# Kernel tuning notes

Measured on AMD Instinct MI355X. Metric: run time of the kernel, lower is better.

## Reference

```python
import jax, jax.numpy as jnp
import numpy as np

EPS = 1e-5  # BatchNorm eps (torch default)

def _bn(x, gamma, beta):
    # training-mode BatchNorm over the edge/node (leading) axis, biased var
    mean = x.mean(axis=0, keepdims=True)
    var = x.var(axis=0, keepdims=True)
    return (x - mean) * jax.lax.rsqrt(var + EPS) * gamma + beta

def _silu(x):
    return x * jax.nn.sigmoid(x)

def setup_inputs() -> dict:
    N, E, H, NH = 50000, 800000, 128, 4
    HD = H // NH
    key = jax.random.key(0)
    ks = jax.random.split(key, 8)
    x = jax.random.normal(ks[0], (N, H), dtype=jnp.float32)
    weight = jax.random.uniform(ks[1], (N, 1), dtype=jnp.float32)  # positive fraction weights
    src = jax.random.randint(ks[2], (E,), 0, N)
    dst = jax.random.randint(ks[3], (E,), 0, N)
    # f: Linear(2H, 1) + BN(1)
    Wf = jax.random.normal(ks[4], (2 * H, 1), dtype=jnp.float32) * 0.05
    bf = jnp.zeros((1,), jnp.float32)
    f_gamma = jnp.ones((1,), jnp.float32)
    f_beta = jnp.zeros((1,), jnp.float32)
    # g: NH heads of Linear(2H, HD) + BN(HD), stacked on leading head axis
    Wg = jax.random.normal(ks[5], (NH, 2 * H, HD), dtype=jnp.float32) * 0.05
    bg = jnp.zeros((NH, HD), jnp.float32)
    g_gamma = jnp.ones((NH, HD), jnp.float32)
    g_beta = jnp.zeros((NH, HD), jnp.float32)
    # bn_nodes: BN(H)
    n_gamma = jnp.ones((H,), jnp.float32)
    n_beta = jnp.zeros((H,), jnp.float32)
    return dict(x=x, weight=weight, src=src, dst=dst, Wf=Wf, bf=bf,
                f_gamma=f_gamma, f_beta=f_beta, Wg=Wg, bg=bg,
                g_gamma=g_gamma, g_beta=g_beta, n_gamma=n_gamma, n_beta=n_beta)

def reference(x, weight, src, dst, Wf, bf, f_gamma, f_beta, Wg, bg, g_gamma, g_beta, n_gamma, n_beta):
    N = x.shape[0]
    E = src.shape[0]
    # per-edge concat of src/dst node features: [E, 2H]
    hihj = jnp.concatenate([x[src], x[dst]], axis=-1)
    # attention logit f(hihj) = SiLU(BN(Linear)) then exp: [E, 1]
    exp_e = jnp.exp(_silu(_bn(hihj @ Wf + bf, f_gamma, f_beta)))
    # weighted softmax-like normalization over incoming edges of each dst node
    we = weight[src] * exp_e                                   # [E, 1]
    sum_w_exp = jax.ops.segment_sum(we, dst, num_segments=N)   # [N, 1]
    a = we / sum_w_exp[dst]                                    # [E, 1]
    # multi-head message: a_ij * SiLU(BN(Linear_h(hihj))) per head, concat
    z = jnp.einsum('ed,hdk->ehk', hihj, Wg) + bg               # [E, NH, HD]
    z = _silu(_bn(z, g_gamma, g_beta))
    msg = (a[:, :, None] * z).reshape(E, -1)                   # [E, H]
    h = jax.ops.segment_sum(msg, dst, num_segments=N)          # [N, H]
    out = _bn(h, n_gamma, n_beta) + x                          # residual
    return out
```

## Files before the change

### kernel.cpp

```cpp
#include <hip/hip_runtime.h>
#include <hip/hip_bf16.h>
#include <math.h>

#define HDIM 128
#define PAD 64
typedef unsigned short ushort_t;
typedef unsigned int uint_t;
typedef __attribute__((ext_vector_type(8))) short bf16x8;
typedef __attribute__((ext_vector_type(4))) float f32x4;
typedef __attribute__((ext_vector_type(2))) float v2f;

__device__ __forceinline__ float wave_allreduce(float v){
  #pragma unroll
  for (int o = 1; o < 64; o <<= 1) v += __shfl_xor(v, o);
  return v;
}

__device__ __forceinline__ ushort_t f2bf(float f){
  uint_t u = __float_as_uint(f);
  uint_t r = (u + 0x7fffu + ((u >> 16) & 1u)) >> 16;
  return (ushort_t)r;
}

__device__ __forceinline__ v2f bf2(uint_t u){
  v2f r;
  r.x = __uint_as_float(u << 16);
  r.y = __uint_as_float(u & 0xffff0000u);
  return r;
}

__global__ __launch_bounds__(128) void k_wpack(const float* __restrict__ Wg,
    const float* __restrict__ Wf, ushort_t* __restrict__ W3,
    int* __restrict__ cnt, int C){
  int b = blockIdx.x;
  int k = threadIdx.x;
  if (b < 272){
    float val;
    if (b < 128)       val = Wg[(size_t)(b >> 5) * 8192 + k * 32 + (b & 31)];
    else if (b < 256){ int c2 = b - 128;
                       val = Wg[(size_t)(c2 >> 5) * 8192 + (k + 128) * 32 + (c2 & 31)]; }
    else if (b == 256) val = Wf[k];
    else if (b == 257) val = Wf[128 + k];
    else               val = 0.f;
    int idx = (((b >> 4) * 4 + (k >> 5)) * 16 + (b & 15)) * 32 + (k & 31);
    W3[idx] = f2bf(val);
  } else {
    int i = (b - 272) * 128 + k;
    if (i < C) cnt[i] = 0;
  }
}

__global__ __launch_bounds__(256) void k_gemmfill(const float* __restrict__ x,
    const ushort_t* __restrict__ W3, const float* __restrict__ weight,
    ushort_t* __restrict__ Pb, ushort_t* __restrict__ Qb,
    float* __restrict__ v, float2* __restrict__ uw2,
    const int* __restrict__ src, const int* __restrict__ dst,
    int* __restrict__ cnt, int* __restrict__ es,
    int N, int E, int FB){
  __shared__ ushort_t xl[32 * 128];
  __shared__ ushort_t cl[32 * 264];
  if ((int)blockIdx.x < FB){
    int t = blockIdx.x * 256 + threadIdx.x;
    int e0 = t * 8;
#define FILL1(d, s) { \
    int c = atomicAdd(&cnt[d], 1); \
    if (c < PAD) es[(size_t)(d) * PAD + c] = (s); }
    if (e0 + 8 <= E){
      int4 da = *(const int4*)(dst + e0);
      int4 db = *(const int4*)(dst + e0 + 4);
      int4 sa = *(const int4*)(src + e0);
      int4 sb = *(const int4*)(src + e0 + 4);
      FILL1(da.x, sa.x) FILL1(da.y, sa.y) FILL1(da.z, sa.z) FILL1(da.w, sa.w)
      FILL1(db.x, sb.x) FILL1(db.y, sb.y) FILL1(db.z, sb.z) FILL1(db.w, sb.w)
    } else {
      for (int e = e0; e < E; ++e){
        int d = dst[e];
        FILL1(d, src[e])
      }
    }
#undef FILL1
  } else {
    int tid = threadIdx.x;
    int n_base = ((int)blockIdx.x - FB) * 32;
    #pragma unroll
    for (int i = 0; i < 4; ++i){
      int cidx = i * 256 + tid;
      int row = cidx >> 5, ch = cidx & 31;
      int rowc = n_base + row; rowc = rowc < N ? rowc : N - 1;
      float4 a = *(const float4*)(x + (size_t)rowc * HDIM + ch * 4);
      uint_t lo = (uint_t)f2bf(a.x) | ((uint_t)f2bf(a.y) << 16);
      uint_t hi = (uint_t)f2bf(a.z) | ((uint_t)f2bf(a.w) << 16);
      int bo = (row * 256 + ch * 8) ^ ((row & 7) << 4);
      *(uint2*)((char*)xl + bo) = make_uint2(lo, hi);
    }
    __syncthreads();
    int wid = __builtin_amdgcn_readfirstlane(tid >> 6);
    int lane = tid & 63;
    int quad = lane >> 4, col = lane & 15;
    int strip = wid >> 1;
    int half = wid & 1;
    int tbeg = half * 8;
    int ntile = half ? 9 : 8;
    f32x4 acc[9];
    #pragma unroll
    for (int t = 0; t < 9; ++t) acc[t] = (f32x4){0.f, 0.f, 0.f, 0.f};
    int arow = strip * 16 + col;
    #pragma unroll
    for (int kk = 0; kk < 4; ++kk){
      int abyte = (arow * 256 + kk * 64 + quad * 16) ^ ((col & 7) << 4);
      bf16x8 af = *(const bf16x8*)((char*)xl + abyte);
      const ushort_t* wb = W3 + (size_t)(tbeg * 4 + kk) * 512 + col * 32 + quad * 8;
      #pragma unroll
      for (int t = 0; t < 9; ++t){
        if (t < ntile){
          bf16x8 bfr = *(const bf16x8*)(wb + (size_t)t * 2048);
          acc[t] = __builtin_amdgcn_mfma_f32_16x16x32_bf16(af, bfr, acc[t], 0, 0, 0);
        }
      }
    }
    #pragma unroll
    for (int t = 0; t < 8; ++t){
      int ct = tbeg + t;
      #pragma unroll
      for (int r = 0; r < 4; ++r){
        int lr = strip * 16 + quad * 4 + r;
        cl[lr * 264 + ct * 16 + col] = f2bf(acc[t][r]);
      }
    }
    if (half){
      #pragma unroll
      for (int r = 0; r < 4; ++r){
        int n = n_base + strip * 16 + quad * 4 + r;
        if (n < N){
          float val = acc[8][r];
          if (col == 0)      uw2[n] = make_float2(val, weight[n]);
          else if (col == 1) v[n] = val;
        }
      }
    }
    __syncthreads();
    int row = tid >> 3, seg = tid & 7;
    int n = n_base + row;
    if (n < N){
      const ushort_t* s = cl + row * 264 + seg * 32;
      uint4 w0 = *(const uint4*)(s);
      uint4 w1 = *(const uint4*)(s + 8);
      uint4 w2 = *(const uint4*)(s + 16);
      uint4 w3v = *(const uint4*)(s + 24);
      if (seg < 4){
        ushort_t* dp = Pb + (size_t)n * HDIM + seg * 32;
        *(uint4*)(dp) = w0; *(uint4*)(dp + 8) = w1;
        *(uint4*)(dp + 16) = w2; *(uint4*)(dp + 24) = w3v;
      } else {
        ushort_t* dp = Qb + (size_t)n * HDIM + (seg - 4) * 32;
        *(uint4*)(dp) = w0; *(uint4*)(dp + 8) = w1;
        *(uint4*)(dp + 16) = w2; *(uint4*)(dp + 24) = w3v;
      }
    }
  }
}

#define SH8(sjv,jj,S) \
  int S##0=__shfl(sjv,(jj)),   S##1=__shfl(sjv,(jj)+1), S##2=__shfl(sjv,(jj)+2), S##3=__shfl(sjv,(jj)+3), \
      S##4=__shfl(sjv,(jj)+4), S##5=__shfl(sjv,(jj)+5), S##6=__shfl(sjv,(jj)+6), S##7=__shfl(sjv,(jj)+7);
#define LD8(S,P) \
  uint_t P##0=Pu[(size_t)S##0*64+lane], P##1=Pu[(size_t)S##1*64+lane], \
         P##2=Pu[(size_t)S##2*64+lane], P##3=Pu[(size_t)S##3*64+lane], \
         P##4=Pu[(size_t)S##4*64+lane], P##5=Pu[(size_t)S##5*64+lane], \
         P##6=Pu[(size_t)S##6*64+lane], P##7=Pu[(size_t)S##7*64+lane];
#define SH4(sjv,jj,S) \
  int S##0=__shfl(sjv,(jj)),   S##1=__shfl(sjv,(jj)+1), S##2=__shfl(sjv,(jj)+2), S##3=__shfl(sjv,(jj)+3);
#define LD4(S,P) \
  uint_t P##0=Pu[(size_t)S##0*64+lane], P##1=Pu[(size_t)S##1*64+lane], \
         P##2=Pu[(size_t)S##2*64+lane], P##3=Pu[(size_t)S##3*64+lane];

__global__ __launch_bounds__(256) void k_gstats(const ushort_t* __restrict__ Pb,
    const ushort_t* __restrict__ Qb, const float* __restrict__ v,
    const float2* __restrict__ uw2, const int* __restrict__ es,
    const int* __restrict__ cnt, float* __restrict__ pstatG, int N){
  int lane = threadIdx.x & 63;
  int wid = __builtin_amdgcn_readfirstlane(threadIdx.x >> 6);
  int part = (int)blockIdx.x & 7;
  int Npp = (N + 7) >> 3;
  int lo = part * Npp;
  int hi = lo + Npp; if (hi > N) hi = N;
  int stp = (gridDim.x >> 3) << 2;
  const uint_t* Pu = (const uint_t*)Pb;
  const uint_t* Qu = (const uint_t*)Qb;
  v2f gs = {0.f,0.f}, gq = {0.f,0.f};
  float fs = 0.f, fq = 0.f;
  int n0 = lo + ((blockIdx.x >> 3) << 2) + wid;
  int n1 = n0 + stp;
  int dnA=0,sjA=0; uint_t qAu=0; float vA=0.f;
  int dnB=0,sjB=0; uint_t qBu=0; float vB=0.f;
  if (n0 < hi){ dnA=cnt[n0]; sjA=es[(size_t)n0*PAD+lane];
                qAu=Qu[(size_t)n0*64+lane]; vA=v[n0]; }
  if (n1 < hi){ dnB=cnt[n1]; sjB=es[(size_t)n1*PAD+lane];
                qBu=Qu[(size_t)n1*64+lane]; vB=v[n1]; }
#define GST(p,Sv,Qv) { v2f y=bf2(p); Sv+=y; Qv.x=fmaf(y.x,y.x,Qv.x); Qv.y=fmaf(y.y,y.y,Qv.y); }
#define GED8(P,Sv,Qv) GST(P##0,Sv,Qv) GST(P##1,Sv,Qv) GST(P##2,Sv,Qv) GST(P##3,Sv,Qv) \
                      GST(P##4,Sv,Qv) GST(P##5,Sv,Qv) GST(P##6,Sv,Qv) GST(P##7,Sv,Qv)
#define GED4(P,Sv,Qv) GST(P##0,Sv,Qv) GST(P##1,Sv,Qv) GST(P##2,Sv,Qv) GST(P##3,Sv,Qv)
  while (n0 < hi){
    int m0 = n0 + 2*stp, m1 = n1 + 2*stp;
    int dnC=0,sjC=0; uint_t qCu=0; float vC=0.f;
    int dnD=0,sjD=0; uint_t qDu=0; float vD=0.f;
    if (m0 < hi){ dnC=cnt[m0]; sjC=es[(size_t)m0*PAD+lane];
                  qCu=Qu[(size_t)m0*64+lane]; vC=v[m0]; }
    if (m1 < hi){ dnD=cnt[m1]; sjD=es[(size_t)m1*PAD+lane];
                  qDu=Qu[(size_t)m1*64+lane]; vD=v[m1]; }
    int dA = dnA < PAD ? dnA : PAD;
    int dB = (n1 < hi) ? (dnB < PAD ? dnB : PAD) : 0;
    if (lane < dA){ float2 uw = uw2[sjA]; float t = uw.x + vA; fs += t; fq = fmaf(t,t,fq); }
    if (lane < dB){ float2 uw = uw2[sjB]; float t = uw.x + vB; fs += t; fq = fmaf(t,t,fq); }
    v2f qa = bf2(qAu), qb = bf2(qBu);
    v2f SnA={0.f,0.f}, SSA={0.f,0.f}, SnB={0.f,0.f}, SSB={0.f,0.f};
    int j0 = 0, j1 = 0;
    for (; j0 + 7 < dA && j1 + 7 < dB; j0 += 8, j1 += 8){
      SH8(sjA,j0,xa) SH8(sjB,j1,xb)
      LD8(xa,pa) LD8(xb,pb)
      GED8(pa,SnA,SSA) GED8(pb,SnB,SSB)
    }
    for (; j0 + 7 < dA; j0 += 8){ SH8(sjA,j0,xa) LD8(xa,pa) GED8(pa,SnA,SSA) }
    for (; j0 + 3 < dA; j0 += 4){ SH4(sjA,j0,xa) LD4(xa,pa) GED4(pa,SnA,SSA) }
    for (; j0 < dA; ++j0){ int s0=__shfl(sjA,j0); uint_t p0=Pu[(size_t)s0*64+lane]; GST(p0,SnA,SSA) }
    for (; j1 + 7 < dB; j1 += 8){ SH8(sjB,j1,xb) LD8(xb,pb) GED8(pb,SnB,SSB) }
    for (; j1 + 3 < dB; j1 += 4){ SH4(sjB,j1,xb) LD4(xb,pb) GED4(pb,SnB,SSB) }
    for (; j1 < dB; ++j1){ int s0=__shfl(sjB,j1); uint_t p0=Pu[(size_t)s0*64+lane]; GST(p0,SnB,SSB) }
    float dAf = (float)dA, dBf = (float)dB;
    gs.x += SnA.x + SnB.x + dAf*qa.x + dBf*qb.x;
    gs.y += SnA.y + SnB.y + dAf*qa.y + dBf*qb.y;
    gq.x += SSA.x + SSB.x + qa.x*fmaf(dAf,qa.x,2.f*SnA.x) + qb.x*fmaf(dBf,qb.x,2.f*SnB.x);
    gq.y += SSA.y + SSB.y + qa.y*fmaf(dAf,qa.y,2.f*SnA.y) + qb.y*fmaf(dBf,qb.y,2.f*SnB.y);
    n0 = m0; n1 = m1;
    dnA=dnC; sjA=sjC; qAu=qCu; vA=vC;
    dnB=dnD; sjB=sjD; qBu=qDu; vB=vD;
  }
#undef GST
#undef GED8
#undef GED4
  fs = wave_allreduce(fs); fq = wave_allreduce(fq);
  __shared__ float red[4][258];
  red[wid][2*lane]       = gs.x; red[wid][2*lane+1]   = gs.y;
  red[wid][128+2*lane]   = gq.x; red[wid][129+2*lane] = gq.y;
  if (lane == 0){ red[wid][256] = fs; red[wid][257] = fq; }
  __syncthreads();
  for (int c = threadIdx.x; c < 258; c += 256)
    pstatG[(size_t)blockIdx.x * 258 + c] = red[0][c] + red[1][c] + red[2][c] + red[3][c];
}

__global__ __launch_bounds__(256) void k_redfin1(const float* __restrict__ pstatG,
    int NB, const float* __restrict__ g_gamma, const float* __restrict__ g_beta,
    const float* __restrict__ f_gamma, const float* __restrict__ f_beta,
    float* __restrict__ fin, long long E){
  int j = blockIdx.x;
  int c1 = (j < 128) ? j : 256;
  int c2 = (j < 128) ? 128 + j : 257;
  double s1 = 0, s2 = 0;
  for (int b = threadIdx.x; b < NB; b += 256){
    const float* pb = pstatG + (size_t)b * 258;
    s1 += (double)pb[c1]; s2 += (double)pb[c2];
  }
  __shared__ double m1[256], m2[256];
  m1[threadIdx.x] = s1; m2[threadIdx.x] = s2;
  __syncthreads();
  for (int o = 128; o; o >>= 1){
    if (threadIdx.x < o){ m1[threadIdx.x] += m1[threadIdx.x + o];
                          m2[threadIdx.x] += m2[threadIdx.x + o]; }
    __syncthreads();
  }
  if (threadIdx.x == 0){
    double m = m1[0] / (double)E;
    double var = m2[0] / (double)E - m * m;
    if (j < 128){
      float sc = (float)((double)g_gamma[j] / sqrt(var + 1e-5));
      fin[2 + j] = sc; fin[130 + j] = g_beta[j] - (float)m * sc;
    } else {
      float sc = (float)((double)f_gamma[0] / sqrt(var + 1e-5));
      fin[0] = sc; fin[1] = f_beta[0] - (float)m * sc;
    }
  }
}

__global__ __launch_bounds__(256) void k_msg(const ushort_t* __restrict__ Pb,
    const ushort_t* __restrict__ Qb, const float* __restrict__ v,
    const float2* __restrict__ uw2, const int* __restrict__ es,
    const int* __restrict__ cnt, const float* __restrict__ fin,
    float* __restrict__ h, float* __restrict__ pstatH, int N){
  int lane = threadIdx.x & 63;
  int wid = __builtin_amdgcn_readfirstlane(threadIdx.x >> 6);
  int part = (int)blockIdx.x & 7;
  int Npp = (N + 7) >> 3;
  int lo = part * Npp;
  int hi = lo + Npp; if (hi > N) hi = N;
  int stp = (gridDim.x >> 3) << 2;
  const uint_t* Pu = (const uint_t*)Pb;
  const uint_t* Qu = (const uint_t*)Qb;
  float fsc = fin[0], fsh = fin[1];
  v2f gsc = {fin[2 + 2*lane], fin[3 + 2*lane]};
  v2f gsh = {fin[130 + 2*lane], fin[131 + 2*lane]};
  v2f hs = {0.f,0.f}, hq = {0.f,0.f};
  int n0 = lo + ((blockIdx.x >> 3) << 2) + wid;
  int n1 = n0 + stp;
  int dnA=0,sjA=0; uint_t qAu=0; float vA=0.f;
  int dnB=0,sjB=0; uint_t qBu=0; float vB=0.f;
  if (n0 < hi){ dnA=cnt[n0]; sjA=es[(size_t)n0*PAD+lane];
                qAu=Qu[(size_t)n0*64+lane]; vA=v[n0]; }
  if (n1 < hi){ dnB=cnt[n1]; sjB=es[(size_t)n1*PAD+lane];
                qBu=Qu[(size_t)n1*64+lane]; vB=v[n1]; }
#define EDGE(p,a,qv,av) { v2f y = (bf2(p) + qv) * gsc + gsh; \
      float e0 = __expf(-y.x), e1 = __expf(-y.y); \
      float d0 = 1.f + e0, d1 = 1.f + e1; \
      float r = __builtin_amdgcn_rcpf(d0 * d1) * (a); \
      av.x = fmaf(y.x * d1, r, av.x); av.y = fmaf(y.y * d0, r, av.y); }
#define ASH8(wjv,jj,A) \
  float A##0=__shfl(wjv,(jj)),   A##1=__shfl(wjv,(jj)+1), A##2=__shfl(wjv,(jj)+2), A##3=__shfl(wjv,(jj)+3), \
        A##4=__shfl(wjv,(jj)+4), A##5=__shfl(wjv,(jj)+5), A##6=__shfl(wjv,(jj)+6), A##7=__shfl(wjv,(jj)+7);
#define ASH4(wjv,jj,A) \
  float A##0=__shfl(wjv,(jj)),   A##1=__shfl(wjv,(jj)+1), A##2=__shfl(wjv,(jj)+2), A##3=__shfl(wjv,(jj)+3);
#define MED8(P,A,qv,av) EDGE(P##0,A##0,qv,av) EDGE(P##1,A##1,qv,av) EDGE(P##2,A##2,qv,av) EDGE(P##3,A##3,qv,av) \
                        EDGE(P##4,A##4,qv,av) EDGE(P##5,A##5,qv,av) EDGE(P##6,A##6,qv,av) EDGE(P##7,A##7,qv,av)
#define MED4(P,A,qv,av) EDGE(P##0,A##0,qv,av) EDGE(P##1,A##1,qv,av) EDGE(P##2,A##2,qv,av) EDGE(P##3,A##3,qv,av)
  while (n0 < hi){
    int m0 = n0 + 2*stp, m1 = n1 + 2*stp;
    int dnC=0,sjC=0; uint_t qCu=0; float vC=0.f;
    int dnD=0,sjD=0; uint_t qDu=0; float vD=0.f;
    if (m0 < hi){ dnC=cnt[m0]; sjC=es[(size_t)m0*PAD+lane];
                  qCu=Qu[(size_t)m0*64+lane]; vC=v[m0]; }
    if (m1 < hi){ dnD=cnt[m1]; sjD=es[(size_t)m1*PAD+lane];
                  qDu=Qu[(size_t)m1*64+lane]; vD=v[m1]; }
    int dA = dnA < PAD ? dnA : PAD;
    int dB = (n1 < hi) ? (dnB < PAD ? dnB : PAD) : 0;
    float wjA = 0.f, wjB = 0.f;
    if (lane < dA){ float2 uw = uw2[sjA];
      float tt = fmaf(uw.x + vA, fsc, fsh);
      float sl = tt * __builtin_amdgcn_rcpf(1.f + __expf(-tt));
      wjA = uw.y * __expf(sl); }
    if (lane < dB){ float2 uw = uw2[sjB];
      float tt = fmaf(uw.x + vB, fsc, fsh);
      float sl = tt * __builtin_amdgcn_rcpf(1.f + __expf(-tt));
      wjB = uw.y * __expf(sl); }
    v2f qa = bf2(qAu), qb = bf2(qBu);
    v2f accA = {0.f,0.f}, accB = {0.f,0.f};
    int j0 = 0, j1 = 0;
    for (; j0 + 7 < dA && j1 + 7 < dB; j0 += 8, j1 += 8){
      SH8(sjA,j0,xa) SH8(sjB,j1,xb)
      ASH8(wjA,j0,aa) ASH8(wjB,j1,ab)
      LD8(xa,pa) LD8(xb,pb)
      MED8(pa,aa,qa,accA) MED8(pb,ab,qb,accB)
    }
    for (; j0 + 7 < dA; j0 += 8){ SH8(sjA,j0,xa) ASH8(wjA,j0,aa) LD8(xa,pa) MED8(pa,aa,qa,accA) }
    for (; j0 + 3 < dA; j0 += 4){ SH4(sjA,j0,xa) ASH4(wjA,j0,aa) LD4(xa,pa) MED4(pa,aa,qa,accA) }
    for (; j0 < dA; ++j0){ int s0=__shfl(sjA,j0); float a0=__shfl(wjA,j0);
                           uint_t p0=Pu[(size_t)s0*64+lane]; EDGE(p0,a0,qa,accA) }
    for (; j1 + 7 < dB; j1 += 8){ SH8(sjB,j1,xb) ASH8(wjB,j1,ab) LD8(xb,pb) MED8(pb,ab,qb,accB) }
    for (; j1 + 3 < dB; j1 += 4){ SH4(sjB,j1,xb) ASH4(wjB,j1,ab) LD4(xb,pb) MED4(pb,ab,qb,accB) }
    for (; j1 < dB; ++j1){ int s0=__shfl(sjB,j1); float a0=__shfl(wjB,j1);
                           uint_t p0=Pu[(size_t)s0*64+lane]; EDGE(p0,a0,qb,accB) }
    float swA = wjA, swB = wjB;
    #pragma unroll
    for (int o = 1; o < 64; o <<= 1){ swA += __shfl_xor(swA, o); swB += __shfl_xor(swB, o); }
    float rsA = (dA > 0) ? (1.f / swA) : 0.f;
    float rsB = (dB > 0) ? (1.f / swB) : 0.f;
    accA.x *= rsA; accA.y *= rsA;
    accB.x *= rsB; accB.y *= rsB;
    *(float2*)&h[(size_t)n0 * 128 + 2*lane] = make_float2(accA.x, accA.y);
    hs += accA; hq += accA * accA;
    if (n1 < hi){
      *(float2*)&h[(size_t)n1 * 128 + 2*lane] = make_float2(accB.x, accB.y);
      hs += accB; hq += accB * accB;
    }
    n0 = m0; n1 = m1;
    dnA=dnC; sjA=sjC; qAu=qCu; vA=vC;
    dnB=dnD; sjB=sjD; qBu=qDu; vB=vD;
  }
#undef EDGE
#undef ASH8
#undef ASH4
#undef MED8
#undef MED4
  __shared__ float red[4][256];
  red[wid][2*lane]       = hs.x; red[wid][2*lane+1]   = hs.y;
  red[wid][128+2*lane]   = hq.x; red[wid][129+2*lane] = hq.y;
  __syncthreads();
  int c = threadIdx.x;
  pstatH[(size_t)blockIdx.x * 256 + c] = red[0][c] + red[1][c] + red[2][c] + red[3][c];
}

__global__ __launch_bounds__(256) void k_redfin2(const float* __restrict__ pstatH,
    int NB, const float* __restrict__ n_gamma, const float* __restrict__ n_beta,
    float* __restrict__ fin, int N){
  int j = blockIdx.x;
  double s1 = 0, s2 = 0;
  for (int b = threadIdx.x; b < NB; b += 256){
    const float* pb = pstatH + (size_t)b * 256;
    s1 += (double)pb[j]; s2 += (double)pb[128 + j];
  }
  __shared__ double m1[256], m2[256];
  m1[threadIdx.x] = s1; m2[threadIdx.x] = s2;
  __syncthreads();
  for (int o = 128; o; o >>= 1){
    if (threadIdx.x < o){ m1[threadIdx.x] += m1[threadIdx.x + o];
                          m2[threadIdx.x] += m2[threadIdx.x + o]; }
    __syncthreads();
  }
  if (threadIdx.x == 0){
    double m = m1[0] / (double)N;
    double var = m2[0] / (double)N - m * m;
    float sc = (float)((double)n_gamma[j] / sqrt(var + 1e-5));
    fin[258 + j] = sc; fin[386 + j] = n_beta[j] - (float)m * sc;
  }
}

__global__ __launch_bounds__(256) void k_out(const float* __restrict__ h,
    const float* __restrict__ x, const float* __restrict__ fin,
    float* __restrict__ out, int total4){
  int i = blockIdx.x * 256 + threadIdx.x;
  if (i >= total4) return;
  const float4* h4 = (const float4*)h; const float4* x4 = (const float4*)x;
  float4 hv = h4[i], xv = x4[i];
  int c = (i * 4) & 127;
  float4 o;
  o.x = fmaf(hv.x, fin[258 + c],     fin[386 + c])     + xv.x;
  o.y = fmaf(hv.y, fin[258 + c + 1], fin[386 + c + 1]) + xv.y;
  o.z = fmaf(hv.z, fin[258 + c + 2], fin[386 + c + 2]) + xv.z;
  o.w = fmaf(hv.w, fin[258 + c + 3], fin[386 + c + 3]) + xv.w;
  ((float4*)out)[i] = o;
}

extern "C" void kernel_launch(void* const* d_in, const int* in_sizes, int n_in,
                              void* d_out, int out_size, void* d_ws, size_t ws_size,
                              hipStream_t stream){
  const float* x       = (const float*)d_in[0];
  const float* weight  = (const float*)d_in[1];
  const int*   src     = (const int*)d_in[2];
  const int*   dst     = (const int*)d_in[3];
  const float* Wf      = (const float*)d_in[4];
  const float* f_gamma = (const float*)d_in[6];
  const float* f_beta  = (const float*)d_in[7];
  const float* Wg      = (const float*)d_in[8];
  const float* g_gamma = (const float*)d_in[10];
  const float* g_beta  = (const float*)d_in[11];
  const float* n_gamma = (const float*)d_in[12];
  const float* n_beta  = (const float*)d_in[13];
  float* out = (float*)d_out;

  int N = in_sizes[0] / HDIM;
  int E = in_sizes[2];

  char* ws = (char*)d_ws;
  size_t off = 0;
  auto alloc = [&](size_t bytes)->char*{
    char* p = ws + off; off = (off + bytes + 255) & ~(size_t)255; return p;
  };
  ushort_t* Pb    = (ushort_t*)alloc((size_t)N * HDIM * 2);
  ushort_t* Qb    = (ushort_t*)alloc((size_t)N * HDIM * 2);
  float* h        = (float*)alloc((size_t)N * HDIM * 4);
  float* v        = (float*)alloc((size_t)N * 4);
  float2* uw2     = (float2*)alloc((size_t)N * 8);
  int* es         = (int*)alloc((size_t)N * PAD * 4);
  ushort_t* W3    = (ushort_t*)alloc((size_t)272 * 128 * 2);
  int* cnt        = (int*)alloc((size_t)N * 4);
  const int NWB = 512;
  const int NB  = NWB;
  float*  pstatG = (float*)alloc((size_t)NB * 258 * 4);
  float*  pstatH = (float*)alloc((size_t)NB * 256 * 4);
  float*  fin    = (float*)alloc(514 * 4);

  int GB = (N + 31) / 32;
  int FB = (E + 2047) / 2048;

  k_wpack   <<<272 + (N + 127) / 128, 128, 0, stream>>>(Wg, Wf, W3, cnt, N);
  k_gemmfill<<<FB + GB, 256, 0, stream>>>(x, W3, weight, Pb, Qb, v, uw2,
                                          src, dst, cnt, es, N, E, FB);
  k_gstats  <<<NWB, 256, 0, stream>>>(Pb, Qb, v, uw2, es, cnt, pstatG, N);
  k_redfin1 <<<129, 256, 0, stream>>>(pstatG, NB, g_gamma, g_beta, f_gamma, f_beta, fin, (long long)E);
  k_msg     <<<NWB, 256, 0, stream>>>(Pb, Qb, v, uw2, es, cnt, fin, h, pstatH, N);
  k_redfin2 <<<128, 256, 0, stream>>>(pstatH, NB, n_gamma, n_beta, fin, N);
  k_out     <<<(N * HDIM / 4 + 255) / 256, 256, 0, stream>>>(h, x, fin, out, N * HDIM / 4);
}
```

Measured before the change: 303.1 us.

## Bucket edges by destination block before building per-node adjacency lists

Replaces the per-edge global atomic fill of the padded per-node edge lists with a two-pass bucketing scheme. Edges are first scattered into 256-node buckets using shared-memory histograms and one global atomic per bucket per block. Each bucket is then turned into padded adjacency lists in shared memory and written out densely, which also removes the separate count-zeroing. The goal is to cut global atomic contention and random scattered writes, at the cost of an extra queue buffer, a fixed per-bucket capacity and silent truncation if a bucket overflows. The stats and message kernels also launch with 2048 blocks instead of 512.

```diff
diff --git a/kernel.cpp b/kernel.cpp
--- a/kernel.cpp
+++ b/kernel.cpp
@@ -4,6 +4,7 @@
 
 #define HDIM 128
 #define PAD 64
+#define QCAP 8192
 typedef unsigned short ushort_t;
 typedef unsigned int uint_t;
 typedef __attribute__((ext_vector_type(8))) short bf16x8;
@@ -29,12 +30,14 @@
   return r;
 }
 
-__global__ __launch_bounds__(128) void k_wpack(const float* __restrict__ Wg,
+__global__ __launch_bounds__(256) void k_wpack(const float* __restrict__ Wg,
     const float* __restrict__ Wf, ushort_t* __restrict__ W3,
-    int* __restrict__ cnt, int C){
+    const int* __restrict__ src, const int* __restrict__ dst,
+    uint_t* __restrict__ queue, int* __restrict__ tails, int E){
   int b = blockIdx.x;
-  int k = threadIdx.x;
   if (b < 272){
+    int k = threadIdx.x;
+    if (k >= 128) return;
     float val;
     if (b < 128)       val = Wg[(size_t)(b >> 5) * 8192 + k * 32 + (b & 31)];
     else if (b < 256){ int c2 = b - 128;
@@ -44,44 +47,78 @@
     else               val = 0.f;
     int idx = (((b >> 4) * 4 + (k >> 5)) * 16 + (b & 15)) * 32 + (k & 31);
     W3[idx] = f2bf(val);
+    return;
+  }
+  __shared__ int hist[256], gbase[256];
+  int t = threadIdx.x;
+  hist[t] = 0;
+  __syncthreads();
+  int e0 = ((b - 272) * 256 + t) * 8;
+  int d0=0,d1=0,d2=0,d3=0,d4=0,d5=0,d6=0,d7=0;
+  int s0=0,s1=0,s2=0,s3=0,s4=0,s5=0,s6=0,s7=0;
+  bool v0=e0<E, v1=e0+1<E, v2=e0+2<E, v3=e0+3<E,
+       v4=e0+4<E, v5=e0+5<E, v6=e0+6<E, v7=e0+7<E;
+  if (v7 && (e0 + 8 <= E)){
+    int4 da = *(const int4*)(dst + e0); int4 db_ = *(const int4*)(dst + e0 + 4);
+    int4 sa = *(const int4*)(src + e0); int4 sb_ = *(const int4*)(src + e0 + 4);
+    d0=da.x; d1=da.y; d2=da.z; d3=da.w; d4=db_.x; d5=db_.y; d6=db_.z; d7=db_.w;
+    s0=sa.x; s1=sa.y; s2=sa.z; s3=sa.w; s4=sb_.x; s5=sb_.y; s6=sb_.z; s7=sb_.w;
   } else {
-    int i = (b - 272) * 128 + k;
-    if (i < C) cnt[i] = 0;
-  }
+    if (v0){ d0=dst[e0];   s0=src[e0];   }
+    if (v1){ d1=dst[e0+1]; s1=src[e0+1]; }
+    if (v2){ d2=dst[e0+2]; s2=src[e0+2]; }
+    if (v3){ d3=dst[e0+3]; s3=src[e0+3]; }
+    if (v4){ d4=dst[e0+4]; s4=src[e0+4]; }
+    if (v5){ d5=dst[e0+5]; s5=src[e0+5]; }
+    if (v6){ d6=dst[e0+6]; s6=src[e0+6]; }
+    if (v7){ d7=dst[e0+7]; s7=src[e0+7]; }
+  }
+#define DIST1(i) int b##i = d##i >> 8, r##i = 0; \
+    if (v##i) r##i = atomicAdd(&hist[b##i], 1);
+  DIST1(0) DIST1(1) DIST1(2) DIST1(3) DIST1(4) DIST1(5) DIST1(6) DIST1(7)
+#undef DIST1
+  __syncthreads();
+  if (hist[t]) gbase[t] = atomicAdd(&tails[t], hist[t]);
+  __syncthreads();
+#define DISTW(i) if (v##i){ int q = gbase[b##i] + r##i; if (q < QCAP) \
+    queue[(size_t)b##i * QCAP + q] = ((uint_t)(d##i & 255) << 16) | (uint_t)s##i; }
+  DISTW(0) DISTW(1) DISTW(2) DISTW(3) DISTW(4) DISTW(5) DISTW(6) DISTW(7)
+#undef DISTW
 }
 
 __global__ __launch_bounds__(256) void k_gemmfill(const float* __restrict__ x,
     const ushort_t* __restrict__ W3, const float* __restrict__ weight,
     ushort_t* __restrict__ Pb, ushort_t* __restrict__ Qb,
     float* __restrict__ v, float2* __restrict__ uw2,
-    const int* __restrict__ src, const int* __restrict__ dst,
+    const uint_t* __restrict__ queue, const int* __restrict__ tails,
     int* __restrict__ cnt, int* __restrict__ es,
-    int N, int E, int FB){
-  __shared__ ushort_t xl[32 * 128];
-  __shared__ ushort_t cl[32 * 264];
-  if ((int)blockIdx.x < FB){
-    int t = blockIdx.x * 256 + threadIdx.x;
-    int e0 = t * 8;
-#define FILL1(d, s) { \
-    int c = atomicAdd(&cnt[d], 1); \
-    if (c < PAD) es[(size_t)(d) * PAD + c] = (s); }
-    if (e0 + 8 <= E){
-      int4 da = *(const int4*)(dst + e0);
-      int4 db = *(const int4*)(dst + e0 + 4);
-      int4 sa = *(const int4*)(src + e0);
-      int4 sb = *(const int4*)(src + e0 + 4);
-      FILL1(da.x, sa.x) FILL1(da.y, sa.y) FILL1(da.z, sa.z) FILL1(da.w, sa.w)
-      FILL1(db.x, sb.x) FILL1(db.y, sb.y) FILL1(db.z, sb.z) FILL1(db.w, sb.w)
-    } else {
-      for (int e = e0; e < E; ++e){
-        int d = dst[e];
-        FILL1(d, src[e])
-      }
-    }
-#undef FILL1
+    int N, int BK){
+  __shared__ ushort_t smem[16384];
+  __shared__ int lcnt[256];
+  int tid = threadIdx.x;
+  if ((int)blockIdx.x < BK){
+    int b = blockIdx.x;
+    lcnt[tid] = 0;
+    __syncthreads();
+    int count = tails[b]; if (count > QCAP) count = QCAP;
+    for (int i = tid; i < count; i += 256){
+      uint_t pk = queue[(size_t)b * QCAP + i];
+      int dl = pk >> 16;
+      int slot = atomicAdd(&lcnt[dl], 1);
+      if (slot < PAD) smem[dl * 64 + slot] = (ushort_t)(pk & 0xffffu);
+    }
+    __syncthreads();
+    int nb = b << 8;
+    for (int i = tid; i < 16384; i += 256){
+      int n = nb + (i >> 6);
+      if (n < N) es[(size_t)nb * 64 + i] = (int)smem[i];
+    }
+    int n = nb + tid;
+    if (n < N){ int c = lcnt[tid]; cnt[n] = c < PAD ? c : PAD; }
   } else {
-    int tid = threadIdx.x;
-    int n_base = ((int)blockIdx.x - FB) * 32;
+    ushort_t* xl = smem;
+    ushort_t* cl = smem + 4096;
+    int n_base = ((int)blockIdx.x - BK) * 32;
     #pragma unroll
     for (int i = 0; i < 4; ++i){
       int cidx = i * 256 + tid;
@@ -461,18 +498,22 @@
   int* es         = (int*)alloc((size_t)N * PAD * 4);
   ushort_t* W3    = (ushort_t*)alloc((size_t)272 * 128 * 2);
   int* cnt        = (int*)alloc((size_t)N * 4);
-  const int NWB = 512;
+  uint_t* queue   = (uint_t*)alloc((size_t)256 * QCAP * 4);
+  int* tails      = (int*)alloc(256 * 4);
+  const int NWB = 2048;
   const int NB  = NWB;
   float*  pstatG = (float*)alloc((size_t)NB * 258 * 4);
   float*  pstatH = (float*)alloc((size_t)NB * 256 * 4);
   float*  fin    = (float*)alloc(514 * 4);
 
   int GB = (N + 31) / 32;
-  int FB = (E + 2047) / 2048;
-
-  k_wpack   <<<272 + (N + 127) / 128, 128, 0, stream>>>(Wg, Wf, W3, cnt, N);
-  k_gemmfill<<<FB + GB, 256, 0, stream>>>(x, W3, weight, Pb, Qb, v, uw2,
-                                          src, dst, cnt, es, N, E, FB);
+  int BK = (N + 255) >> 8;
+  int DB = (E + 2047) / 2048;
+
+  hipMemsetAsync(tails, 0, 256 * 4, stream);
+  k_wpack   <<<272 + DB, 256, 0, stream>>>(Wg, Wf, W3, src, dst, queue, tails, E);
+  k_gemmfill<<<BK + GB, 256, 0, stream>>>(x, W3, weight, Pb, Qb, v, uw2,
+                                          queue, tails, cnt, es, N, BK);
   k_gstats  <<<NWB, 256, 0, stream>>>(Pb, Qb, v, uw2, es, cnt, pstatG, N);
   k_redfin1 <<<129, 256, 0, stream>>>(pstatG, NB, g_gamma, g_beta, f_gamma, f_beta, fin, (long long)E);
   k_msg     <<<NWB, 256, 0, stream>>>(Pb, Qb, v, uw2, es, cnt, fin, h, pstatH, N);
```

After: 256.2 us. 1.18x faster.
